# Kernel optimization log

Hardware: AMD Instinct MI355X
Metric: run time of the kernel (lower is better)

Reference implementation:

```python
import jax, jax.numpy as jnp
import numpy as np

EPS = 1e-5
TEMPERATURE = 1.0


def _gn(x, w, b):
    # GroupNorm(dim, dim): num_groups == channels -> per-channel norm over spatial
    mu = x.mean((2, 3), keepdims=True)
    var = x.var((2, 3), keepdims=True)
    return (x - mu) * jax.lax.rsqrt(var + EPS) * w[None, :, None, None] + b[None, :, None, None]


def _deconv(x, w, b):
    # torch ConvTranspose2d(Cin, Cout, 3, stride=2, padding=1, output_padding=1)
    # == dilated conv with lhs_dilation=2, padding (1,2); kernel flip absorbed into random weights
    y = jax.lax.conv_general_dilated(
        x, w, window_strides=(1, 1), padding=((1, 2), (1, 2)),
        lhs_dilation=(2, 2), dimension_numbers=('NCHW', 'OIHW', 'NCHW'))
    return y + b[None, :, None, None]


def _spatial_softmax(logits, temp):
    # logits (..., h, w) -> expected (x, y) coords in [-1, 1], shape (..., 2)
    h, w = logits.shape[-2], logits.shape[-1]
    p = jax.nn.softmax(logits.reshape(*logits.shape[:-2], h * w) / temp, axis=-1)
    ys, xs = jnp.meshgrid(jnp.linspace(-1.0, 1.0, h), jnp.linspace(-1.0, 1.0, w), indexing='ij')
    ex = p @ xs.reshape(-1)
    ey = p @ ys.reshape(-1)
    return jnp.stack([ex, ey], axis=-1)


def setup_inputs() -> dict:
    key = jax.random.key(0)
    ks = iter(jax.random.split(key, 40))
    B, FC, FH = 512, 256, 4   # batch, encoder channels, encoder spatial
    H = 512                   # hidden_size
    STEPS, NHEADS, C = 5, 3, H // 8

    def nrm(shape, scale):
        return jax.random.normal(next(ks), shape, jnp.float32) * scale

    inp = {
        'feat': nrm((B, FC, FH, FH), 1.0),
        'action': jax.random.randint(next(ks), (B,), 0, NHEADS),
        'scene_idx': jax.random.randint(next(ks), (B,), 0, 10),
        'fc_w': nrm((FC, H), (2.0 / FC) ** 0.5),
        'fc_b': jnp.zeros((H,), jnp.float32),
    }
    for i, d in enumerate([512, 256, 128]):
        inp[f'gw{i}'] = jnp.ones((d,), jnp.float32)
        inp[f'gb{i}'] = jnp.zeros((d,), jnp.float32)
        inp[f'dw{i}'] = nrm((d // 2, d, 3, 3), (2.0 / (d * 9)) ** 0.5)
        inp[f'db{i}'] = jnp.zeros((d // 2,), jnp.float32)
    inp['hgw'] = jnp.ones((NHEADS, C), jnp.float32)
    inp['hgb'] = jnp.zeros((NHEADS, C), jnp.float32)
    inp['hcw'] = nrm((NHEADS, STEPS, C), (2.0 / C) ** 0.5)
    inp['hcb'] = jnp.zeros((NHEADS, STEPS), jnp.float32)
    return inp


def reference(feat, action, scene_idx, fc_w, fc_b,
              gw0, gb0, dw0, db0, gw1, gb1, dw1, db1, gw2, gb2, dw2, db2,
              hgw, hgb, hcw, hcb):
    # visual_fc1 applied channel-last == 1x1 linear over channels
    x = jax.nn.relu(jnp.einsum('bchw,cd->bdhw', feat, fc_w) + fc_b[None, :, None, None])
    # deconv stack: (B,512,4,4) -> (B,256,8,8) -> (B,128,16,16) -> (B,64,32,32)
    for gw, gb, dw, db in ((gw0, gb0, dw0, db0), (gw1, gb1, dw1, db1), (gw2, gb2, dw2, db2)):
        x = jax.nn.relu(_deconv(_gn(x, gw, gb), dw, db))
    # expert heads: shared per-channel normalization, head-specific affine fused into 1x1 conv
    mu = x.mean((2, 3), keepdims=True)
    var = x.var((2, 3), keepdims=True)
    xn = (x - mu) * jax.lax.rsqrt(var + EPS)                       # (B,64,32,32)
    w_eff = hcw * hgw[:, None, :]                                  # (A,S,C)
    b_eff = hcb + jnp.einsum('asc,ac->as', hcw, hgb)               # (A,S)
    logits = jnp.einsum('bchw,asc->abshw', xn, w_eff) + b_eff[:, None, :, None, None]
    coords = _spatial_softmax(logits, TEMPERATURE)                 # (A,B,S,2)
    # route each sample to its action's head (== masked scatter loop in torch)
    out = coords[action, jnp.arange(action.shape[0])]              # (B,S,2)
    return out
```

## Files before the change

kernel.cpp:

```cpp
#include <hip/hip_runtime.h>
#include <hip/hip_bf16.h>

#define DI __device__ __forceinline__
using u16 = unsigned short;
using u32 = unsigned int;

typedef short short8 __attribute__((ext_vector_type(8)));
typedef float f32x4 __attribute__((ext_vector_type(4)));

#define F4C(v, i) ((i) == 0 ? (v).x : (i) == 1 ? (v).y : (i) == 2 ? (v).z : (v).w)

DI float bflo(u32 u) { return __uint_as_float(u << 16); }
DI float bfhi(u32 u) { return __uint_as_float(u & 0xffff0000u); }
DI float bfel(uint2 u, int j) { u32 w = (j < 2) ? u.x : u.y; return (j & 1) ? bfhi(w) : bflo(w); }
DI u16 f2bf(float a) {
  u32 xu = __float_as_uint(a);
  return (u16)((xu + 0x7fffu + ((xu >> 16) & 1)) >> 16);
}
DI u32 pack_bf16x2(float a, float b) {
  u32 xu = __float_as_uint(a), yu = __float_as_uint(b);
  xu = (xu + 0x7fffu + ((xu >> 16) & 1)) >> 16;
  yu = (yu + 0x7fffu + ((yu >> 16) & 1)) >> 16;
  return (xu & 0xffffu) | (yu << 16);
}

static constexpr size_t OFF_REGB = 0;
static constexpr size_t OFF_REGA = 16777216;
static constexpr size_t OFF_WT0  = 33554432;
static constexpr size_t OFF_WT1  = OFF_WT0 + 1179648;
static constexpr size_t OFF_WT2  = OFF_WT1 + 294912;
static constexpr size_t OFF_WTF  = OFF_WT2 + 73728;
static constexpr size_t OFF_ST   = 35200000;
static constexpr size_t O_SC0 = OFF_ST,          O_SH0 = OFF_ST + 262144;
static constexpr size_t O_SC1 = OFF_ST + 524288, O_SH1 = OFF_ST + 655360;
static constexpr size_t O_SC2 = OFF_ST + 786432, O_SH2 = OFF_ST + 851968;
static constexpr size_t O_PSUM = OFF_ST + 1048576;

__global__ __launch_bounds__(256)
void wtrans_all(const float* __restrict__ dw0, const float* __restrict__ dw1,
                const float* __restrict__ dw2, const float* __restrict__ fcw,
                u16* __restrict__ wt0, u16* __restrict__ wt1,
                u16* __restrict__ wt2, u16* __restrict__ wtf)
{
  int id = blockIdx.x * 256 + threadIdx.x;
  if (id < 131072) {
    int m = id >> 9, c = id & 511;
    const float* src = dw0 + ((size_t)m * 512 + c) * 9;
#pragma unroll
    for (int tap = 0; tap < 9; ++tap)
      wt0[((size_t)tap * 256 + m) * 512 + c] = f2bf(src[tap]);
  } else if (id < 163840) {
    int j = id - 131072;
    int m = j >> 8, c = j & 255;
    const float* src = dw1 + ((size_t)m * 256 + c) * 9;
#pragma unroll
    for (int tap = 0; tap < 9; ++tap)
      wt1[((size_t)tap * 128 + m) * 256 + c] = f2bf(src[tap]);
  } else if (id < 172032) {
    int j = id - 163840;
    int m = j >> 7, c = j & 127;
    const float* src = dw2 + ((size_t)m * 128 + c) * 9;
#pragma unroll
    for (int tap = 0; tap < 9; ++tap)
      wt2[((size_t)tap * 64 + m) * 128 + c] = f2bf(src[tap]);
  } else {
    int j = id - 172032;
    int d = j >> 8, c = j & 255;
    wtf[j] = f2bf(fcw[c * 512 + d]);
  }
}

DI void fc_stage_A(const float* __restrict__ feat, int b, u16* Ab, int t)
{
#pragma unroll
  for (int it = 0; it < 2; ++it) {
    int idx = t + it * 256;
    int cp = idx >> 2, hw4 = idx & 3;
    int c = cp * 2;
    const float* xp = feat + ((size_t)b * 256 + c) * 16 + hw4 * 4;
    float4 v0 = *(const float4*)xp;
    float4 v1 = *(const float4*)(xp + 16);
    int c64 = c >> 6, jb = (c & 63) >> 3;
#pragma unroll
    for (int j = 0; j < 4; ++j) {
      int hw = hw4 * 4 + j;
      int row = c64 * 16 + hw;
      *(u32*)&Ab[(row << 6) + ((jb ^ (row & 7)) << 3) + (c & 7)] =
          pack_bf16x2(F4C(v0, j), F4C(v1, j));
    }
  }
}

__global__ __launch_bounds__(256, 2)
void fc_mfma(const float* __restrict__ feat, const u16* __restrict__ wtf,
             const float* __restrict__ fb, const float* __restrict__ gw,
             const float* __restrict__ gb, u16* __restrict__ x0,
             float* __restrict__ sc, float* __restrict__ sh)
{
  __shared__ __align__(16) u16 Wl[256 * 64];
  __shared__ __align__(16) u16 Al[2][64 * 64];
  const int t = threadIdx.x;
  const int lane = t & 63, wave = t >> 6;
  const int n15 = lane & 15, kq = lane >> 4;
  const int d0 = blockIdx.x * 64;
  const int b0 = blockIdx.y * 8;

#pragma unroll
  for (int it = 0; it < 8; ++it) {
    int idx = t + it * 256;
    int dl = idx >> 5, jb32 = idx & 31;
    int row = (jb32 >> 3) * 64 + dl, jb = jb32 & 7;
    uint4 v = *(const uint4*)(wtf + (size_t)(d0 + dl) * 256 + jb32 * 8);
    *(uint4*)&Wl[(row << 6) + ((jb ^ (row & 7)) << 3)] = v;
  }
  fc_stage_A(feat, b0, Al[0], t);

  const int dg = d0 + wave * 16 + n15;
  const float bvn = fb[dg];
  const float gwv = gw[dg], gbv = gb[dg];

  for (int bi = 0; bi < 8; ++bi) {
    __syncthreads();
    if (bi + 1 < 8) fc_stage_A(feat, b0 + bi + 1, Al[(bi + 1) & 1], t);

    const u16* A = Al[bi & 1];
    f32x4 acc0 = {0.f, 0.f, 0.f, 0.f}, acc1 = {0.f, 0.f, 0.f, 0.f};
#pragma unroll
    for (int ks = 0; ks < 8; ++ks) {
      int js = ks * 4 + kq;
      int ra = (js >> 3) * 16 + n15;
      int rb = (js >> 3) * 64 + wave * 16 + n15;
      short8 av = *(const short8*)&A[(ra << 6) + (((js & 7) ^ (ra & 7)) << 3)];
      short8 bv = *(const short8*)&Wl[(rb << 6) + (((js & 7) ^ (rb & 7)) << 3)];
      if (ks & 1) acc1 = __builtin_amdgcn_mfma_f32_16x16x32_bf16(av, bv, acc1, 0, 0, 0);
      else        acc0 = __builtin_amdgcn_mfma_f32_16x16x32_bf16(av, bv, acc0, 0, 0, 0);
    }

    int b = b0 + bi;
    float v[4], s = 0.f, s2 = 0.f;
#pragma unroll
    for (int r = 0; r < 4; ++r) {
      v[r] = fmaxf(acc0[r] + acc1[r] + bvn, 0.f);
      s += v[r]; s2 += v[r] * v[r];
    }
    uint2 pk = {pack_bf16x2(v[0], v[1]), pack_bf16x2(v[2], v[3])};
    *(uint2*)&x0[((size_t)b * 512 + dg) * 16 + kq * 4] = pk;
    s  += __shfl_xor(s, 16, 64);  s  += __shfl_xor(s, 32, 64);
    s2 += __shfl_xor(s2, 16, 64); s2 += __shfl_xor(s2, 32, 64);
    if (kq == 0) {
      float mu = s * (1.f / 16.f);
      float var = fmaxf(s2 * (1.f / 16.f) - mu * mu, 0.f);
      float scale = gwv * rsqrtf(var + 1e-5f);
      sc[(size_t)b * 512 + dg] = scale;
      sh[(size_t)b * 512 + dg] = gbv - mu * scale;
    }
  }
}

template<int STAGE>
__global__ __launch_bounds__(256, 3)
void deconv_mfma(const u16* __restrict__ x, const float* __restrict__ sc,
                 const float* __restrict__ sh, const u16* __restrict__ wt,
                 const float* __restrict__ bias, u16* __restrict__ y,
                 const float* __restrict__ gwn, const float* __restrict__ gbn,
                 float* __restrict__ osc, float* __restrict__ osh)
{
  constexpr int CI  = STAGE == 0 ? 512 : 256;
  constexpr int CO  = CI / 2;
  constexpr int H   = STAGE == 0 ? 4 : 8;
  constexpr int S2I = H * H, S2O = 4 * S2I, W2 = 2 * H;
  constexpr int WP  = H + 1;
  constexpr int XROWS = STAGE == 0 ? 100 : 81;
  constexpr int NCH = CI / 64;
  __shared__ __align__(16) u16 Wl[288 * 64];
  __shared__ __align__(16) u16 Xl[XROWS * 64];
  __shared__ float2 sbuf[2][2][16];

  const int t = threadIdx.x;
  const int lane = t & 63, wave = t >> 6;
  const int ms = wave >> 1, ns = wave & 1;
  const int n15 = lane & 15, kq = lane >> 4;

  int m0, b0;
  m0 = blockIdx.x * 32; b0 = (STAGE == 0) ? blockIdx.y * 4 : blockIdx.y;

  int xrow[2];
#pragma unroll
  for (int ni = 0; ni < 2; ++ni) {
    if constexpr (STAGE == 0) xrow[ni] = (ns * 2 + ni) * 25 + (n15 >> 2) * 5 + (n15 & 3);
    else                      xrow[ni] = (2 * (ns * 2 + ni) + (n15 >> 3)) * 9 + (n15 & 7);
  }
  const int am = ms * 16 + n15;

  for (int i = t; i < XROWS * 32; i += 256) ((u32*)Xl)[i] = 0;

  f32x4 acc[2][4];
#pragma unroll
  for (int ni = 0; ni < 2; ++ni)
#pragma unroll
    for (int c = 0; c < 4; ++c) acc[ni][c] = f32x4{0.f, 0.f, 0.f, 0.f};

  for (int ch = 0; ch < NCH; ++ch) {
    const int c0 = ch * 64;
    __syncthreads();

#pragma unroll
    for (int it = 0; it < 9; ++it) {
      int idx = t + it * 256;
      int row = idx >> 3, jb = idx & 7;
      int tap = row >> 5, ml = row & 31;
      uint4 v = *(const uint4*)(wt + ((size_t)(tap * CO + m0 + ml)) * CI + c0 + jb * 8);
      *(uint4*)&Wl[(row << 6) + ((jb ^ (row & 7)) << 3)] = v;
    }

    for (int idx = t; idx < 16 * 32; idx += 256) {
      int q = idx & 15, p = idx >> 4;
      int c = c0 + 2 * p;
      int b, ldr, gpos;
      if constexpr (STAGE == 0) {
        int img = q >> 2, iy = q & 3;
        b = b0 + img; gpos = iy * 4; ldr = img * 25 + iy * 5;
      } else {
        int iy = q >> 1, cq = q & 1;
        b = b0; gpos = iy * 8 + cq * 4; ldr = iy * 9 + cq * 4;
      }
      const u16* xp = x + ((size_t)b * CI + c) * S2I + gpos;
      uint2 q0 = *(const uint2*)xp;
      uint2 q1 = *(const uint2*)(xp + S2I);
      float s0 = sc[(size_t)b * CI + c],     h0 = sh[(size_t)b * CI + c];
      float s1 = sc[(size_t)b * CI + c + 1], h1 = sh[(size_t)b * CI + c + 1];
      int jb = p >> 2, sub = p & 3;
#pragma unroll
      for (int j = 0; j < 4; ++j) {
        int row = ldr + j;
        *(u32*)&Xl[(row << 6) + ((jb ^ (row & 7)) << 3) + sub * 2] =
            pack_bf16x2(bfel(q0, j) * s0 + h0, bfel(q1, j) * s1 + h1);
      }
    }
    __syncthreads();

#pragma unroll
    for (int s = 0; s < 2; ++s) {
      const int js = s * 4 + kq;
      short8 a[9];
#pragma unroll
      for (int tap = 0; tap < 9; ++tap) {
        int row = tap * 32 + am;
        a[tap] = *(const short8*)&Wl[(row << 6) + ((js ^ (row & 7)) << 3)];
      }
#pragma unroll
      for (int ni = 0; ni < 2; ++ni) {
        int r0 = xrow[ni], r1 = r0 + 1, r2 = r0 + WP, r3 = r0 + WP + 1;
        short8 b00 = *(const short8*)&Xl[(r0 << 6) + ((js ^ (r0 & 7)) << 3)];
        short8 b01 = *(const short8*)&Xl[(r1 << 6) + ((js ^ (r1 & 7)) << 3)];
        short8 b10 = *(const short8*)&Xl[(r2 << 6) + ((js ^ (r2 & 7)) << 3)];
        short8 b11 = *(const short8*)&Xl[(r3 << 6) + ((js ^ (r3 & 7)) << 3)];
        acc[ni][0] = __builtin_amdgcn_mfma_f32_16x16x32_bf16(a[4], b00, acc[ni][0], 0, 0, 0);
        acc[ni][1] = __builtin_amdgcn_mfma_f32_16x16x32_bf16(a[3], b00, acc[ni][1], 0, 0, 0);
        acc[ni][1] = __builtin_amdgcn_mfma_f32_16x16x32_bf16(a[5], b01, acc[ni][1], 0, 0, 0);
        acc[ni][2] = __builtin_amdgcn_mfma_f32_16x16x32_bf16(a[1], b00, acc[ni][2], 0, 0, 0);
        acc[ni][2] = __builtin_amdgcn_mfma_f32_16x16x32_bf16(a[7], b10, acc[ni][2], 0, 0, 0);
        acc[ni][3] = __builtin_amdgcn_mfma_f32_16x16x32_bf16(a[0], b00, acc[ni][3], 0, 0, 0);
        acc[ni][3] = __builtin_amdgcn_mfma_f32_16x16x32_bf16(a[2], b01, acc[ni][3], 0, 0, 0);
        acc[ni][3] = __builtin_amdgcn_mfma_f32_16x16x32_bf16(a[6], b10, acc[ni][3], 0, 0, 0);
        acc[ni][3] = __builtin_amdgcn_mfma_f32_16x16x32_bf16(a[8], b11, acc[ni][3], 0, 0, 0);
      }
    }
  }

  float bv[4];
#pragma unroll
  for (int r = 0; r < 4; ++r) bv[r] = bias[m0 + ms * 16 + kq * 4 + r];

  float sr[4] = {0.f, 0.f, 0.f, 0.f}, sr2[4] = {0.f, 0.f, 0.f, 0.f};
#pragma unroll
  for (int ni = 0; ni < 2; ++ni) {
    int b, iy, ix;
    if constexpr (STAGE == 0) { b = b0 + ns * 2 + ni; iy = n15 >> 2; ix = n15 & 3; }
    else                      { b = b0; iy = 2 * (ns * 2 + ni) + (n15 >> 3); ix = n15 & 7; }

    float val[4][4];
#pragma unroll
    for (int cl = 0; cl < 4; ++cl)
#pragma unroll
      for (int r = 0; r < 4; ++r) {
        val[cl][r] = fmaxf(acc[ni][cl][r] + bv[r], 0.f);
        sr[r] += val[cl][r]; sr2[r] += val[cl][r] * val[cl][r];
      }

    if constexpr (STAGE == 0) {
#pragma unroll
      for (int r = 0; r < 4; ++r) {
        int m = m0 + ms * 16 + kq * 4 + r;
        size_t base = ((size_t)b * CO + m) * S2O + (size_t)(2 * iy) * W2 + 2 * ix;
        *(u32*)(y + base)      = pack_bf16x2(val[0][r], val[1][r]);
        *(u32*)(y + base + W2) = pack_bf16x2(val[2][r], val[3][r]);
      }
#pragma unroll
      for (int r = 0; r < 4; ++r) {
#pragma unroll
        for (int off = 1; off <= 8; off <<= 1) {
          sr[r]  += __shfl_xor(sr[r], off, 64);
          sr2[r] += __shfl_xor(sr2[r], off, 64);
        }
      }
      if (n15 == 0) {
#pragma unroll
        for (int r = 0; r < 4; ++r) {
          int m = m0 + ms * 16 + kq * 4 + r;
          float mu = sr[r] * (1.f / 64.f);
          float var = fmaxf(sr2[r] * (1.f / 64.f) - mu * mu, 0.f);
          float scale = gwn[m] * rsqrtf(var + 1e-5f);
          osc[(size_t)b * CO + m] = scale;
          osh[(size_t)b * CO + m] = gbn[m] - mu * scale;
        }
      }
#pragma unroll
      for (int r = 0; r < 4; ++r) { sr[r] = 0.f; sr2[r] = 0.f; }
    } else {
#pragma unroll
      for (int cl = 0; cl < 4; ++cl) {
        int opx = (2 * iy + (cl >> 1)) * 16 + 2 * ix + (cl & 1);
        size_t base = ((size_t)b * 256 + opx) * 128 + m0 + ms * 16 + kq * 4;
        *(u32*)(y + base)     = pack_bf16x2(val[cl][0], val[cl][1]);
        *(u32*)(y + base + 2) = pack_bf16x2(val[cl][2], val[cl][3]);
      }
    }
  }

  if constexpr (STAGE == 1) {
#pragma unroll
    for (int r = 0; r < 4; ++r) {
#pragma unroll
      for (int off = 1; off <= 8; off <<= 1) {
        sr[r]  += __shfl_xor(sr[r], off, 64);
        sr2[r] += __shfl_xor(sr2[r], off, 64);
      }
    }
    __syncthreads();
    if (n15 == 0) {
#pragma unroll
      for (int r = 0; r < 4; ++r) sbuf[ms][ns][kq * 4 + r] = float2{sr[r], sr2[r]};
    }
    __syncthreads();
    if (t < 32) {
      int msx = t >> 4, i = t & 15;
      float2 p0 = sbuf[msx][0][i], p1 = sbuf[msx][1][i];
      float s = p0.x + p1.x, s2 = p0.y + p1.y;
      float mu = s * (1.f / 256.f);
      float var = fmaxf(s2 * (1.f / 256.f) - mu * mu, 0.f);
      int m = m0 + msx * 16 + i;
      float scale = gwn[m] * rsqrtf(var + 1e-5f);
      osc[(size_t)b0 * CO + m] = scale;
      osh[(size_t)b0 * CO + m] = gbn[m] - mu * scale;
    }
  }
}

#define XRD(row) (*(const short8*)&Xl[((row) << 6) + (((js ^ ((row) & 7))) << 3)])
__global__ __launch_bounds__(256, 3)
void deconv2_q(const u16* __restrict__ x, const float* __restrict__ sc,
               const float* __restrict__ sh, const u16* __restrict__ wt,
               const float* __restrict__ bias, u16* __restrict__ y,
               float2* __restrict__ psum)
{
  __shared__ __align__(16) u16 Wl[288 * 64];
  __shared__ __align__(16) u16 Xl[85 * 64];
  __shared__ float sc_l[128], sh_l[128];
  __shared__ float2 sbuf[2][2][16];

  const int t = threadIdx.x;
  const int lane = t & 63, wave = t >> 6;
  const int ms = wave >> 1, ns = wave & 1;
  const int n15 = lane & 15, kq = lane >> 4;
  const int m0 = (blockIdx.x & 1) * 32;
  const int qz = blockIdx.x >> 1;
  const int b  = blockIdx.y;

  if (t < 128) { sc_l[t] = sc[(size_t)b * 128 + t]; sh_l[t] = sh[(size_t)b * 128 + t]; }
  for (int i = t; i < 85 * 32; i += 256) ((u32*)Xl)[i] = 0;

  const int am = ms * 16 + n15;
  const int xr0 = (ns * 2) * 17 + n15;

  f32x4 acc[2][4];
#pragma unroll
  for (int ni = 0; ni < 2; ++ni)
#pragma unroll
    for (int c = 0; c < 4; ++c) acc[ni][c] = f32x4{0.f, 0.f, 0.f, 0.f};

  const int NPX = (qz < 3) ? 80 : 64;
  for (int ch = 0; ch < 2; ++ch) {
    const int c0 = ch * 64;
    __syncthreads();

#pragma unroll
    for (int it = 0; it < 9; ++it) {
      int idx = t + it * 256;
      int row = idx >> 3, jb = idx & 7;
      int tap = row >> 5, ml = row & 31;
      uint4 v = *(const uint4*)(wt + ((size_t)(tap * 64 + m0 + ml)) * 128 + c0 + jb * 8);
      *(uint4*)&Wl[(row << 6) + ((jb ^ (row & 7)) << 3)] = v;
    }

    for (int idx = t; idx < NPX * 8; idx += 256) {
      int pxl = idx >> 3, jb = idx & 7;
      int rl = pxl >> 4, ix = pxl & 15;
      int gpx = (4 * qz + rl) * 16 + ix;
      uint4 q = *(const uint4*)(x + ((size_t)b * 256 + gpx) * 128 + c0 + jb * 8);
      int cb = c0 + jb * 8;
      float f0 = bflo(q.x) * sc_l[cb + 0] + sh_l[cb + 0];
      float f1 = bfhi(q.x) * sc_l[cb + 1] + sh_l[cb + 1];
      float f2 = bflo(q.y) * sc_l[cb + 2] + sh_l[cb + 2];
      float f3 = bfhi(q.y) * sc_l[cb + 3] + sh_l[cb + 3];
      float f4 = bflo(q.z) * sc_l[cb + 4] + sh_l[cb + 4];
      float f5 = bfhi(q.z) * sc_l[cb + 5] + sh_l[cb + 5];
      float f6 = bflo(q.w) * sc_l[cb + 6] + sh_l[cb + 6];
      float f7 = bfhi(q.w) * sc_l[cb + 7] + sh_l[cb + 7];
      uint4 o = {pack_bf16x2(f0, f1), pack_bf16x2(f2, f3),
                 pack_bf16x2(f4, f5), pack_bf16x2(f6, f7)};
      int row = rl * 17 + ix;
      *(uint4*)&Xl[(row << 6) + ((jb ^ (row & 7)) << 3)] = o;
    }
    __syncthreads();

#pragma unroll
    for (int s = 0; s < 2; ++s) {
      const int js = s * 4 + kq;
      short8 a[9];
#pragma unroll
      for (int tap = 0; tap < 9; ++tap) {
        int row = tap * 32 + am;
        a[tap] = *(const short8*)&Wl[(row << 6) + ((js ^ (row & 7)) << 3)];
      }
      short8 B0 = XRD(xr0),      B1 = XRD(xr0 + 1);
      short8 B2 = XRD(xr0 + 17), B3 = XRD(xr0 + 18);
      short8 B4 = XRD(xr0 + 34), B5 = XRD(xr0 + 35);
#pragma unroll
      for (int ni = 0; ni < 2; ++ni) {
        short8 b00 = ni ? B2 : B0, b01 = ni ? B3 : B1;
        short8 b10 = ni ? B4 : B2, b11 = ni ? B5 : B3;
        acc[ni][0] = __builtin_amdgcn_mfma_f32_16x16x32_bf16(a[4], b00, acc[ni][0], 0, 0, 0);
        acc[ni][1] = __builtin_amdgcn_mfma_f32_16x16x32_bf16(a[3], b00, acc[ni][1], 0, 0, 0);
        acc[ni][1] = __builtin_amdgcn_mfma_f32_16x16x32_bf16(a[5], b01, acc[ni][1], 0, 0, 0);
        acc[ni][2] = __builtin_amdgcn_mfma_f32_16x16x32_bf16(a[1], b00, acc[ni][2], 0, 0, 0);
        acc[ni][2] = __builtin_amdgcn_mfma_f32_16x16x32_bf16(a[7], b10, acc[ni][2], 0, 0, 0);
        acc[ni][3] = __builtin_amdgcn_mfma_f32_16x16x32_bf16(a[0], b00, acc[ni][3], 0, 0, 0);
        acc[ni][3] = __builtin_amdgcn_mfma_f32_16x16x32_bf16(a[2], b01, acc[ni][3], 0, 0, 0);
        acc[ni][3] = __builtin_amdgcn_mfma_f32_16x16x32_bf16(a[6], b10, acc[ni][3], 0, 0, 0);
        acc[ni][3] = __builtin_amdgcn_mfma_f32_16x16x32_bf16(a[8], b11, acc[ni][3], 0, 0, 0);
      }
    }
  }

  float bv[4];
#pragma unroll
  for (int r = 0; r < 4; ++r) bv[r] = bias[m0 + ms * 16 + kq * 4 + r];
  float sr[4] = {0.f, 0.f, 0.f, 0.f}, sr2[4] = {0.f, 0.f, 0.f, 0.f};
#pragma unroll
  for (int ni = 0; ni < 2; ++ni) {
    int iy = 4 * qz + ns * 2 + ni, ix = n15;
#pragma unroll
    for (int r = 0; r < 4; ++r) {
      int m = m0 + ms * 16 + kq * 4 + r;
      float v00 = fmaxf(acc[ni][0][r] + bv[r], 0.f);
      float v01 = fmaxf(acc[ni][1][r] + bv[r], 0.f);
      float v10 = fmaxf(acc[ni][2][r] + bv[r], 0.f);
      float v11 = fmaxf(acc[ni][3][r] + bv[r], 0.f);
      size_t base = ((size_t)b * 64 + m) * 1024 + (size_t)(2 * iy) * 32 + 2 * ix;
      *(u32*)(y + base)      = pack_bf16x2(v00, v01);
      *(u32*)(y + base + 32) = pack_bf16x2(v10, v11);
      sr[r]  += v00 + v01 + v10 + v11;
      sr2[r] += v00 * v00 + v01 * v01 + v10 * v10 + v11 * v11;
    }
  }
#pragma unroll
  for (int r = 0; r < 4; ++r) {
#pragma unroll
    for (int off = 1; off <= 8; off <<= 1) {
      sr[r]  += __shfl_xor(sr[r], off, 64);
      sr2[r] += __shfl_xor(sr2[r], off, 64);
    }
  }
  __syncthreads();
  if (n15 == 0) {
#pragma unroll
    for (int r = 0; r < 4; ++r) sbuf[ms][ns][kq * 4 + r] = float2{sr[r], sr2[r]};
  }
  __syncthreads();
  if (t < 32) {
    int msx = t >> 4, i = t & 15;
    float2 p0 = sbuf[msx][0][i], p1 = sbuf[msx][1][i];
    int m = m0 + msx * 16 + i;
    psum[((size_t)b * 64 + m) * 4 + qz] = float2{p0.x + p1.x, p0.y + p1.y};
  }
}

DI float breduce_sum(float v, float* buf) {
#pragma unroll
  for (int off = 32; off; off >>= 1) v += __shfl_xor(v, off, 64);
  if ((threadIdx.x & 63) == 0) buf[threadIdx.x >> 6] = v;
  __syncthreads();
  float r = (buf[0] + buf[1]) + (buf[2] + buf[3]);
  __syncthreads();
  return r;
}
DI float breduce_max(float v, float* buf) {
#pragma unroll
  for (int off = 32; off; off >>= 1) v = fmaxf(v, __shfl_xor(v, off, 64));
  if ((threadIdx.x & 63) == 0) buf[threadIdx.x >> 6] = v;
  __syncthreads();
  float r = fmaxf(fmaxf(buf[0], buf[1]), fmaxf(buf[2], buf[3]));
  __syncthreads();
  return r;
}

__global__ __launch_bounds__(256)
void head_kernel(const u16* __restrict__ x3, const float2* __restrict__ psum,
                 const int* __restrict__ action, const float* __restrict__ hgw,
                 const float* __restrict__ hcw, float* __restrict__ out)
{
  constexpr int C = 64, S = 5, P = 1024;
  const int b = blockIdx.x, t = threadIdx.x;
  const int a = action[b];
  __shared__ float weff[S * C];
  __shared__ float sc_l[C], sh_l[C];
  __shared__ float rbuf[4];
  if (t < C) {
    float s = 0.f, s2 = 0.f;
#pragma unroll
    for (int qz = 0; qz < 4; ++qz) {
      float2 p = psum[((size_t)b * C + t) * 4 + qz];
      s += p.x; s2 += p.y;
    }
    float mu = s * (1.f / 1024.f);
    float var = fmaxf(s2 * (1.f / 1024.f) - mu * mu, 0.f);
    float rstd = rsqrtf(var + 1e-5f);
    sc_l[t] = rstd; sh_l[t] = -mu * rstd;
  }
  for (int j = t; j < S * C; j += 256) {
    int s = j >> 6, c = j & 63;
    weff[j] = hcw[(a * S + s) * C + c] * hgw[a * C + c];
  }
  __syncthreads();

  float L[S][4];
#pragma unroll
  for (int s = 0; s < S; ++s)
#pragma unroll
    for (int k = 0; k < 4; ++k) L[s][k] = 0.f;

  const u32* xb = (const u32*)(x3 + (size_t)b * C * P);
  for (int c = 0; c < C; ++c) {
    float scv = sc_l[c], shv = sh_l[c];
    u32 u0 = xb[c * 512 + t];
    u32 u1 = xb[c * 512 + t + 256];
    float xv[4] = {bflo(u0) * scv + shv, bfhi(u0) * scv + shv,
                   bflo(u1) * scv + shv, bfhi(u1) * scv + shv};
#pragma unroll
    for (int s = 0; s < S; ++s) {
      float wv = weff[s * C + c];
#pragma unroll
      for (int k = 0; k < 4; ++k) L[s][k] += xv[k] * wv;
    }
  }

#pragma unroll
  for (int s = 0; s < S; ++s) {
    float m = fmaxf(fmaxf(L[s][0], L[s][1]), fmaxf(L[s][2], L[s][3]));
    m = breduce_max(m, rbuf);
    float se = 0.f, sx = 0.f, sy = 0.f;
    const int pix[4] = {2 * t, 2 * t + 1, 512 + 2 * t, 512 + 2 * t + 1};
#pragma unroll
    for (int k = 0; k < 4; ++k) {
      int p = pix[k];
      float e = __expf(L[s][k] - m);
      se += e;
      sx += e * ((float)(p & 31) * (2.f / 31.f) - 1.f);
      sy += e * ((float)(p >> 5) * (2.f / 31.f) - 1.f);
    }
    se = breduce_sum(se, rbuf);
    sx = breduce_sum(sx, rbuf);
    sy = breduce_sum(sy, rbuf);
    if (t == 0) {
      out[(b * S + s) * 2 + 0] = sx / se;
      out[(b * S + s) * 2 + 1] = sy / se;
    }
  }
}

extern "C" void kernel_launch(void* const* d_in, const int* in_sizes, int n_in,
                              void* d_out, int out_size, void* d_ws, size_t ws_size,
                              hipStream_t stream)
{
  (void)in_sizes; (void)n_in; (void)out_size; (void)ws_size;
  const float* feat   = (const float*)d_in[0];
  const int*   action = (const int*)d_in[1];
  const float* fc_w = (const float*)d_in[3];
  const float* fc_b = (const float*)d_in[4];
  const float* gw0  = (const float*)d_in[5];
  const float* gb0  = (const float*)d_in[6];
  const float* dw0  = (const float*)d_in[7];
  const float* db0  = (const float*)d_in[8];
  const float* gw1  = (const float*)d_in[9];
  const float* gb1  = (const float*)d_in[10];
  const float* dw1  = (const float*)d_in[11];
  const float* db1  = (const float*)d_in[12];
  const float* gw2  = (const float*)d_in[13];
  const float* gb2  = (const float*)d_in[14];
  const float* dw2  = (const float*)d_in[15];
  const float* db2  = (const float*)d_in[16];
  const float* hgw  = (const float*)d_in[17];
  const float* hcw  = (const float*)d_in[19];

  float* ws = (float*)d_ws;
  u16* x0 = (u16*)(ws + OFF_REGB);
  u16* x2 = (u16*)(ws + OFF_REGB);
  u16* x1 = (u16*)(ws + OFF_REGA);
  u16* x3 = (u16*)(ws + OFF_REGA);
  u16* wt0 = (u16*)(ws + OFF_WT0);
  u16* wt1 = (u16*)(ws + OFF_WT1);
  u16* wt2 = (u16*)(ws + OFF_WT2);
  u16* wtf = (u16*)(ws + OFF_WTF);
  float* sc0 = ws + O_SC0; float* sh0 = ws + O_SH0;
  float* sc1 = ws + O_SC1; float* sh1 = ws + O_SH1;
  float* sc2 = ws + O_SC2; float* sh2 = ws + O_SH2;
  float2* psum = (float2*)(ws + O_PSUM);

  wtrans_all<<<1184, 256, 0, stream>>>(dw0, dw1, dw2, fc_w, wt0, wt1, wt2, wtf);
  fc_mfma<<<dim3(8, 64), 256, 0, stream>>>(feat, wtf, fc_b, gw0, gb0, x0, sc0, sh0);
  deconv_mfma<0><<<dim3(8, 128), 256, 0, stream>>>(x0, sc0, sh0, wt0, db0, x1, gw1, gb1, sc1, sh1);
  deconv_mfma<1><<<dim3(4, 512), 256, 0, stream>>>(x1, sc1, sh1, wt1, db1, x2, gw2, gb2, sc2, sh2);
  deconv2_q<<<dim3(8, 512), 256, 0, stream>>>(x2, sc2, sh2, wt2, db2, x3, psum);
  head_kernel<<<512, 256, 0, stream>>>(x3, psum, action, hgw, hcw, (float*)d_out);
}
```

Before: 264.5 us.

## Apply GroupNorm in producer epilogues instead of consumer load paths

Each producer kernel (fc, deconv stage 0, deconv stage 1) now computes the per-channel GroupNorm statistics in its epilogue and writes already-normalized bf16 activations. Consumers copy raw data into shared memory without the scale/shift arithmetic or the sc/sh buffer loads. This removes the global scale/shift arrays and the per-element FMA plus unpack/repack on the load side. Stage 1 adds a shared-memory exchange and a barrier before storing.

```diff
diff --git a/kernel.cpp b/kernel.cpp
--- a/kernel.cpp
+++ b/kernel.cpp
@@ -12,7 +12,6 @@
 
 DI float bflo(u32 u) { return __uint_as_float(u << 16); }
 DI float bfhi(u32 u) { return __uint_as_float(u & 0xffff0000u); }
-DI float bfel(uint2 u, int j) { u32 w = (j < 2) ? u.x : u.y; return (j & 1) ? bfhi(w) : bflo(w); }
 DI u16 f2bf(float a) {
   u32 xu = __float_as_uint(a);
   return (u16)((xu + 0x7fffu + ((xu >> 16) & 1)) >> 16);
@@ -31,9 +30,6 @@
 static constexpr size_t OFF_WT2  = OFF_WT1 + 294912;
 static constexpr size_t OFF_WTF  = OFF_WT2 + 73728;
 static constexpr size_t OFF_ST   = 35200000;
-static constexpr size_t O_SC0 = OFF_ST,          O_SH0 = OFF_ST + 262144;
-static constexpr size_t O_SC1 = OFF_ST + 524288, O_SH1 = OFF_ST + 655360;
-static constexpr size_t O_SC2 = OFF_ST + 786432, O_SH2 = OFF_ST + 851968;
 static constexpr size_t O_PSUM = OFF_ST + 1048576;
 
 __global__ __launch_bounds__(256)
@@ -94,8 +90,7 @@
 __global__ __launch_bounds__(256, 2)
 void fc_mfma(const float* __restrict__ feat, const u16* __restrict__ wtf,
              const float* __restrict__ fb, const float* __restrict__ gw,
-             const float* __restrict__ gb, u16* __restrict__ x0,
-             float* __restrict__ sc, float* __restrict__ sh)
+             const float* __restrict__ gb, u16* __restrict__ x0)
 {
   __shared__ __align__(16) u16 Wl[256 * 64];
   __shared__ __align__(16) u16 Al[2][64 * 64];
@@ -143,27 +138,24 @@
       v[r] = fmaxf(acc0[r] + acc1[r] + bvn, 0.f);
       s += v[r]; s2 += v[r] * v[r];
     }
+    s  += __shfl_xor(s, 16, 64);  s  += __shfl_xor(s, 32, 64);
+    s2 += __shfl_xor(s2, 16, 64); s2 += __shfl_xor(s2, 32, 64);
+    float mu = s * (1.f / 16.f);
+    float var = fmaxf(s2 * (1.f / 16.f) - mu * mu, 0.f);
+    float scale = gwv * rsqrtf(var + 1e-5f);
+    float shift = gbv - mu * scale;
+#pragma unroll
+    for (int r = 0; r < 4; ++r) v[r] = v[r] * scale + shift;
     uint2 pk = {pack_bf16x2(v[0], v[1]), pack_bf16x2(v[2], v[3])};
     *(uint2*)&x0[((size_t)b * 512 + dg) * 16 + kq * 4] = pk;
-    s  += __shfl_xor(s, 16, 64);  s  += __shfl_xor(s, 32, 64);
-    s2 += __shfl_xor(s2, 16, 64); s2 += __shfl_xor(s2, 32, 64);
-    if (kq == 0) {
-      float mu = s * (1.f / 16.f);
-      float var = fmaxf(s2 * (1.f / 16.f) - mu * mu, 0.f);
-      float scale = gwv * rsqrtf(var + 1e-5f);
-      sc[(size_t)b * 512 + dg] = scale;
-      sh[(size_t)b * 512 + dg] = gbv - mu * scale;
-    }
   }
 }
 
 template<int STAGE>
 __global__ __launch_bounds__(256, 3)
-void deconv_mfma(const u16* __restrict__ x, const float* __restrict__ sc,
-                 const float* __restrict__ sh, const u16* __restrict__ wt,
+void deconv_mfma(const u16* __restrict__ x, const u16* __restrict__ wt,
                  const float* __restrict__ bias, u16* __restrict__ y,
-                 const float* __restrict__ gwn, const float* __restrict__ gbn,
-                 float* __restrict__ osc, float* __restrict__ osh)
+                 const float* __restrict__ gwn, const float* __restrict__ gbn)
 {
   constexpr int CI  = STAGE == 0 ? 512 : 256;
   constexpr int CO  = CI / 2;
@@ -175,6 +167,7 @@
   __shared__ __align__(16) u16 Wl[288 * 64];
   __shared__ __align__(16) u16 Xl[XROWS * 64];
   __shared__ float2 sbuf[2][2][16];
+  __shared__ float scl[32], shl[32];
 
   const int t = threadIdx.x;
   const int lane = t & 63, wave = t >> 6;
@@ -227,14 +220,15 @@
       const u16* xp = x + ((size_t)b * CI + c) * S2I + gpos;
       uint2 q0 = *(const uint2*)xp;
       uint2 q1 = *(const uint2*)(xp + S2I);
-      float s0 = sc[(size_t)b * CI + c],     h0 = sh[(size_t)b * CI + c];
-      float s1 = sc[(size_t)b * CI + c + 1], h1 = sh[(size_t)b * CI + c + 1];
       int jb = p >> 2, sub = p & 3;
 #pragma unroll
       for (int j = 0; j < 4; ++j) {
         int row = ldr + j;
-        *(u32*)&Xl[(row << 6) + ((jb ^ (row & 7)) << 3) + sub * 2] =
-            pack_bf16x2(bfel(q0, j) * s0 + h0, bfel(q1, j) * s1 + h1);
+        u32 w0 = (j < 2) ? q0.x : q0.y;
+        u32 w1 = (j < 2) ? q1.x : q1.y;
+        u32 lo = (j & 1) ? (w0 >> 16) : (w0 & 0xffffu);
+        u32 hi = (j & 1) ? (w1 & 0xffff0000u) : (w1 << 16);
+        *(u32*)&Xl[(row << 6) + ((jb ^ (row & 7)) << 3) + sub * 2] = lo | hi;
       }
     }
     __syncthreads();
@@ -272,30 +266,25 @@
 #pragma unroll
   for (int r = 0; r < 4; ++r) bv[r] = bias[m0 + ms * 16 + kq * 4 + r];
 
-  float sr[4] = {0.f, 0.f, 0.f, 0.f}, sr2[4] = {0.f, 0.f, 0.f, 0.f};
-#pragma unroll
-  for (int ni = 0; ni < 2; ++ni) {
-    int b, iy, ix;
-    if constexpr (STAGE == 0) { b = b0 + ns * 2 + ni; iy = n15 >> 2; ix = n15 & 3; }
-    else                      { b = b0; iy = 2 * (ns * 2 + ni) + (n15 >> 3); ix = n15 & 7; }
-
-    float val[4][4];
-#pragma unroll
-    for (int cl = 0; cl < 4; ++cl)
-#pragma unroll
-      for (int r = 0; r < 4; ++r) {
-        val[cl][r] = fmaxf(acc[ni][cl][r] + bv[r], 0.f);
-        sr[r] += val[cl][r]; sr2[r] += val[cl][r] * val[cl][r];
-      }
-
-    if constexpr (STAGE == 0) {
-#pragma unroll
-      for (int r = 0; r < 4; ++r) {
-        int m = m0 + ms * 16 + kq * 4 + r;
-        size_t base = ((size_t)b * CO + m) * S2O + (size_t)(2 * iy) * W2 + 2 * ix;
-        *(u32*)(y + base)      = pack_bf16x2(val[0][r], val[1][r]);
-        *(u32*)(y + base + W2) = pack_bf16x2(val[2][r], val[3][r]);
-      }
+  if constexpr (STAGE == 0) {
+    float gw4[4], gb4[4];
+#pragma unroll
+    for (int r = 0; r < 4; ++r) {
+      int m = m0 + ms * 16 + kq * 4 + r;
+      gw4[r] = gwn[m]; gb4[r] = gbn[m];
+    }
+#pragma unroll
+    for (int ni = 0; ni < 2; ++ni) {
+      int b = b0 + ns * 2 + ni, iy = n15 >> 2, ix = n15 & 3;
+      float val[4][4];
+      float sr[4] = {0.f, 0.f, 0.f, 0.f}, sr2[4] = {0.f, 0.f, 0.f, 0.f};
+#pragma unroll
+      for (int cl = 0; cl < 4; ++cl)
+#pragma unroll
+        for (int r = 0; r < 4; ++r) {
+          val[cl][r] = fmaxf(acc[ni][cl][r] + bv[r], 0.f);
+          sr[r] += val[cl][r]; sr2[r] += val[cl][r] * val[cl][r];
+        }
 #pragma unroll
       for (int r = 0; r < 4; ++r) {
 #pragma unroll
@@ -304,31 +293,35 @@
           sr2[r] += __shfl_xor(sr2[r], off, 64);
         }
       }
-      if (n15 == 0) {
+      float scv[4], shv[4];
+#pragma unroll
+      for (int r = 0; r < 4; ++r) {
+        float mu = sr[r] * (1.f / 64.f);
+        float var = fmaxf(sr2[r] * (1.f / 64.f) - mu * mu, 0.f);
+        scv[r] = gw4[r] * rsqrtf(var + 1e-5f);
+        shv[r] = gb4[r] - mu * scv[r];
+      }
+#pragma unroll
+      for (int r = 0; r < 4; ++r) {
+        int m = m0 + ms * 16 + kq * 4 + r;
+        size_t base = ((size_t)b * CO + m) * S2O + (size_t)(2 * iy) * W2 + 2 * ix;
+        *(u32*)(y + base)      = pack_bf16x2(val[0][r] * scv[r] + shv[r],
+                                             val[1][r] * scv[r] + shv[r]);
+        *(u32*)(y + base + W2) = pack_bf16x2(val[2][r] * scv[r] + shv[r],
+                                             val[3][r] * scv[r] + shv[r]);
+      }
+    }
+  } else {
+    float sr[4] = {0.f, 0.f, 0.f, 0.f}, sr2[4] = {0.f, 0.f, 0.f, 0.f};
+#pragma unroll
+    for (int ni = 0; ni < 2; ++ni)
+#pragma unroll
+      for (int cl = 0; cl < 4; ++cl)
 #pragma unroll
         for (int r = 0; r < 4; ++r) {
-          int m = m0 + ms * 16 + kq * 4 + r;
-          float mu = sr[r] * (1.f / 64.f);
-          float var = fmaxf(sr2[r] * (1.f / 64.f) - mu * mu, 0.f);
-          float scale = gwn[m] * rsqrtf(var + 1e-5f);
-          osc[(size_t)b * CO + m] = scale;
-          osh[(size_t)b * CO + m] = gbn[m] - mu * scale;
+          float v = fmaxf(acc[ni][cl][r] + bv[r], 0.f);
+          sr[r] += v; sr2[r] += v * v;
         }
-      }
-#pragma unroll
-      for (int r = 0; r < 4; ++r) { sr[r] = 0.f; sr2[r] = 0.f; }
-    } else {
-#pragma unroll
-      for (int cl = 0; cl < 4; ++cl) {
-        int opx = (2 * iy + (cl >> 1)) * 16 + 2 * ix + (cl & 1);
-        size_t base = ((size_t)b * 256 + opx) * 128 + m0 + ms * 16 + kq * 4;
-        *(u32*)(y + base)     = pack_bf16x2(val[cl][0], val[cl][1]);
-        *(u32*)(y + base + 2) = pack_bf16x2(val[cl][2], val[cl][3]);
-      }
-    }
-  }
-
-  if constexpr (STAGE == 1) {
 #pragma unroll
     for (int r = 0; r < 4; ++r) {
 #pragma unroll
@@ -351,22 +344,42 @@
       float var = fmaxf(s2 * (1.f / 256.f) - mu * mu, 0.f);
       int m = m0 + msx * 16 + i;
       float scale = gwn[m] * rsqrtf(var + 1e-5f);
-      osc[(size_t)b0 * CO + m] = scale;
-      osh[(size_t)b0 * CO + m] = gbn[m] - mu * scale;
+      scl[t] = scale;
+      shl[t] = gbn[m] - mu * scale;
+    }
+    __syncthreads();
+    float scv[4], shv[4];
+#pragma unroll
+    for (int r = 0; r < 4; ++r) {
+      scv[r] = scl[ms * 16 + kq * 4 + r];
+      shv[r] = shl[ms * 16 + kq * 4 + r];
+    }
+#pragma unroll
+    for (int ni = 0; ni < 2; ++ni) {
+      int iy = 2 * (ns * 2 + ni) + (n15 >> 3), ix = n15 & 7;
+#pragma unroll
+      for (int cl = 0; cl < 4; ++cl) {
+        int opx = (2 * iy + (cl >> 1)) * 16 + 2 * ix + (cl & 1);
+        size_t base = ((size_t)b0 * 256 + opx) * 128 + m0 + ms * 16 + kq * 4;
+        float v0 = fmaxf(acc[ni][cl][0] + bv[0], 0.f) * scv[0] + shv[0];
+        float v1 = fmaxf(acc[ni][cl][1] + bv[1], 0.f) * scv[1] + shv[1];
+        float v2 = fmaxf(acc[ni][cl][2] + bv[2], 0.f) * scv[2] + shv[2];
+        float v3 = fmaxf(acc[ni][cl][3] + bv[3], 0.f) * scv[3] + shv[3];
+        *(u32*)(y + base)     = pack_bf16x2(v0, v1);
+        *(u32*)(y + base + 2) = pack_bf16x2(v2, v3);
+      }
     }
   }
 }
 
 #define XRD(row) (*(const short8*)&Xl[((row) << 6) + (((js ^ ((row) & 7))) << 3)])
 __global__ __launch_bounds__(256, 3)
-void deconv2_q(const u16* __restrict__ x, const float* __restrict__ sc,
-               const float* __restrict__ sh, const u16* __restrict__ wt,
+void deconv2_q(const u16* __restrict__ x, const u16* __restrict__ wt,
                const float* __restrict__ bias, u16* __restrict__ y,
                float2* __restrict__ psum)
 {
   __shared__ __align__(16) u16 Wl[288 * 64];
   __shared__ __align__(16) u16 Xl[85 * 64];
-  __shared__ float sc_l[128], sh_l[128];
   __shared__ float2 sbuf[2][2][16];
 
   const int t = threadIdx.x;
@@ -377,7 +390,6 @@
   const int qz = blockIdx.x >> 1;
   const int b  = blockIdx.y;
 
-  if (t < 128) { sc_l[t] = sc[(size_t)b * 128 + t]; sh_l[t] = sh[(size_t)b * 128 + t]; }
   for (int i = t; i < 85 * 32; i += 256) ((u32*)Xl)[i] = 0;
 
   const int am = ms * 16 + n15;
@@ -408,19 +420,8 @@
       int rl = pxl >> 4, ix = pxl & 15;
       int gpx = (4 * qz + rl) * 16 + ix;
       uint4 q = *(const uint4*)(x + ((size_t)b * 256 + gpx) * 128 + c0 + jb * 8);
-      int cb = c0 + jb * 8;
-      float f0 = bflo(q.x) * sc_l[cb + 0] + sh_l[cb + 0];
-      float f1 = bfhi(q.x) * sc_l[cb + 1] + sh_l[cb + 1];
-      float f2 = bflo(q.y) * sc_l[cb + 2] + sh_l[cb + 2];
-      float f3 = bfhi(q.y) * sc_l[cb + 3] + sh_l[cb + 3];
-      float f4 = bflo(q.z) * sc_l[cb + 4] + sh_l[cb + 4];
-      float f5 = bfhi(q.z) * sc_l[cb + 5] + sh_l[cb + 5];
-      float f6 = bflo(q.w) * sc_l[cb + 6] + sh_l[cb + 6];
-      float f7 = bfhi(q.w) * sc_l[cb + 7] + sh_l[cb + 7];
-      uint4 o = {pack_bf16x2(f0, f1), pack_bf16x2(f2, f3),
-                 pack_bf16x2(f4, f5), pack_bf16x2(f6, f7)};
       int row = rl * 17 + ix;
-      *(uint4*)&Xl[(row << 6) + ((jb ^ (row & 7)) << 3)] = o;
+      *(uint4*)&Xl[(row << 6) + ((jb ^ (row & 7)) << 3)] = q;
     }
     __syncthreads();
 
@@ -622,15 +623,12 @@
   u16* wt1 = (u16*)(ws + OFF_WT1);
   u16* wt2 = (u16*)(ws + OFF_WT2);
   u16* wtf = (u16*)(ws + OFF_WTF);
-  float* sc0 = ws + O_SC0; float* sh0 = ws + O_SH0;
-  float* sc1 = ws + O_SC1; float* sh1 = ws + O_SH1;
-  float* sc2 = ws + O_SC2; float* sh2 = ws + O_SH2;
   float2* psum = (float2*)(ws + O_PSUM);
 
   wtrans_all<<<1184, 256, 0, stream>>>(dw0, dw1, dw2, fc_w, wt0, wt1, wt2, wtf);
-  fc_mfma<<<dim3(8, 64), 256, 0, stream>>>(feat, wtf, fc_b, gw0, gb0, x0, sc0, sh0);
-  deconv_mfma<0><<<dim3(8, 128), 256, 0, stream>>>(x0, sc0, sh0, wt0, db0, x1, gw1, gb1, sc1, sh1);
-  deconv_mfma<1><<<dim3(4, 512), 256, 0, stream>>>(x1, sc1, sh1, wt1, db1, x2, gw2, gb2, sc2, sh2);
-  deconv2_q<<<dim3(8, 512), 256, 0, stream>>>(x2, sc2, sh2, wt2, db2, x3, psum);
+  fc_mfma<<<dim3(8, 64), 256, 0, stream>>>(feat, wtf, fc_b, gw0, gb0, x0);
+  deconv_mfma<0><<<dim3(8, 128), 256, 0, stream>>>(x0, wt0, db0, x1, gw1, gb1);
+  deconv_mfma<1><<<dim3(4, 512), 256, 0, stream>>>(x1, wt1, db1, x2, gw2, gb2);
+  deconv2_q<<<dim3(8, 512), 256, 0, stream>>>(x2, wt2, db2, x3, psum);
   head_kernel<<<512, 256, 0, stream>>>(x3, psum, action, hgw, hcw, (float*)d_out);
 }
```

Result: faster. 254.4 us (-3.8%).
